# Kernel tuning notes

Measured on AMD Instinct MI355X. Metric: run time of the kernel, lower is better.

The kernel has to match this reference:

```python
import jax, jax.numpy as jnp
import numpy as np
import math

EMB_DIM = 1024
N_HEADS = 16
HEAD_DIM = EMB_DIM // N_HEADS
B, T = 4, 2048


def bitlinear(x, w):
    # BitNet b1.58 absmean ternary quantization. NOTE: the source never
    # rescales the ternary weights by `scale`, so forward uses raw {-1,0,1}.
    scale = jnp.maximum(jnp.mean(jnp.abs(w)), 1e-8)
    w_ternary = jnp.clip(jnp.round(w / scale), -1.0, 1.0)
    w_q = w + jax.lax.stop_gradient(w_ternary - w)  # STE
    return x @ w_q.T


def setup_inputs() -> dict:
    key = jax.random.key(0)
    k1, k2, k3 = jax.random.split(key, 3)
    x = jax.random.normal(k1, (B, T, EMB_DIM), dtype=jnp.float32)
    w_qkv = jax.random.normal(k2, (3 * EMB_DIM, EMB_DIM), dtype=jnp.float32) * 0.02
    w_out = jax.random.normal(k3, (EMB_DIM, EMB_DIM), dtype=jnp.float32) * 0.02
    return {"x": x, "w_qkv": w_qkv, "w_out": w_out}


def reference(x, w_qkv, w_out):
    Bc, Tc, C = x.shape
    qkv = bitlinear(x, w_qkv)  # [B, T, 3C]
    q, k, v = jnp.split(qkv, 3, axis=2)

    def split_heads(t):  # [B, T, C] -> [B, H, T, D]
        return t.reshape(Bc, Tc, N_HEADS, HEAD_DIM).transpose(0, 2, 1, 3)

    q, k, v = split_heads(q), split_heads(k), split_heads(v)
    scale = math.sqrt(HEAD_DIM)
    scores = jnp.einsum("bhqd,bhkd->bhqk", q, k) / scale  # [B, H, T, T]
    causal = jnp.triu(jnp.ones((Tc, Tc), dtype=bool), k=1)
    scores = jnp.where(causal, -jnp.inf, scores)
    attn = jax.nn.softmax(scores, axis=-1)
    out = jnp.einsum("bhqk,bhkd->bhqd", attn, v)  # [B, H, T, D]
    out = out.transpose(0, 2, 1, 3).reshape(Bc, Tc, C)
    return bitlinear(out, w_out)
```

## Files before the change

kernel.cpp:

```cpp
#include <hip/hip_runtime.h>
#include <hip/hip_bf16.h>

#define EMB   1024
#define NHEAD 16
#define HDIM  64
#define BSZ   4
#define SEQ   2048
#define MROWS (BSZ*SEQ)
#define NQKV  (3*EMB)

typedef __bf16 bf16;
typedef __bf16 bf16v4 __attribute__((ext_vector_type(4)));
typedef __bf16 bf16v8 __attribute__((ext_vector_type(8)));
typedef float  f32v4  __attribute__((ext_vector_type(4)));
typedef float  f32v16 __attribute__((ext_vector_type(16)));
typedef int    i32v4  __attribute__((ext_vector_type(4)));
typedef int    i32v16 __attribute__((ext_vector_type(16)));
typedef char   c8v4   __attribute__((ext_vector_type(4)));

#define MFMA16(a,b,c)   __builtin_amdgcn_mfma_f32_16x16x32_bf16((a),(b),(c),0,0,0)
#define MFMA32B(a,b,c)  __builtin_amdgcn_mfma_f32_32x32x16_bf16((a),(b),(c),0,0,0)
#define MFMAI8_32(a,b,c) __builtin_amdgcn_mfma_i32_32x32x32_i8((a),(b),(c),0,0,0)

__device__ __forceinline__ void gload_lds16(const void* g, void* l) {
  __builtin_amdgcn_global_load_lds((const __attribute__((address_space(1))) void*)g,
                                   (__attribute__((address_space(3))) void*)l,
                                   16, 0, 0);
}

#define DPP_FMAX(x, ctrl) do {                                                     \
    int _t = __builtin_amdgcn_update_dpp(0, __float_as_int(x), (ctrl), 0xf, 0xf, true); \
    (x) = fmaxf((x), __int_as_float(_t)); } while (0)


__global__ void abs_sum_kernel(const float4* __restrict__ w, int n4, float* out) {
  float s = 0.f;
  for (int i = blockIdx.x * blockDim.x + threadIdx.x; i < n4; i += gridDim.x * blockDim.x) {
    float4 v = w[i];
    s += fabsf(v.x) + fabsf(v.y) + fabsf(v.z) + fabsf(v.w);
  }
  #pragma unroll
  for (int off = 32; off; off >>= 1) s += __shfl_down(s, off, 64);
  __shared__ float red[4];
  int lane = threadIdx.x & 63, wid = threadIdx.x >> 6;
  if (lane == 0) red[wid] = s;
  __syncthreads();
  if (threadIdx.x == 0) atomicAdd(out, red[0] + red[1] + red[2] + red[3]);
}

__global__ void ternarize_both_kernel(const float4* __restrict__ wqkv,
                                      const float4* __restrict__ wout,
                                      const float* __restrict__ sums,
                                      c8v4* __restrict__ out8,
                                      bf16v4* __restrict__ outb) {
  int i = blockIdx.x * blockDim.x + threadIdx.x;
  const int N1_4 = (NQKV * EMB) / 4;
  if (i < N1_4) {
    float scale = fmaxf(sums[0] / (float)(NQKV * EMB), 1e-8f);
    float4 v = wqkv[i];
    c8v4 o;
    o[0] = (char)(int)fmaxf(-1.f, fminf(1.f, rintf(v.x / scale)));
    o[1] = (char)(int)fmaxf(-1.f, fminf(1.f, rintf(v.y / scale)));
    o[2] = (char)(int)fmaxf(-1.f, fminf(1.f, rintf(v.z / scale)));
    o[3] = (char)(int)fmaxf(-1.f, fminf(1.f, rintf(v.w / scale)));
    out8[i] = o;
  } else {
    int j = i - N1_4;
    float scale = fmaxf(sums[1] / (float)(EMB * EMB), 1e-8f);
    float4 v = wout[j];
    bf16v4 o;
    o[0] = (bf16)fmaxf(-1.f, fminf(1.f, rintf(v.x / scale)));
    o[1] = (bf16)fmaxf(-1.f, fminf(1.f, rintf(v.y / scale)));
    o[2] = (bf16)fmaxf(-1.f, fminf(1.f, rintf(v.z / scale)));
    o[3] = (bf16)fmaxf(-1.f, fminf(1.f, rintf(v.w / scale)));
    outb[j] = o;
  }
}

__global__ void quant_x_kernel(const float4* __restrict__ x, c8v4* __restrict__ p1,
                               c8v4* __restrict__ p2, int n4) {
  int i = blockIdx.x * blockDim.x + threadIdx.x;
  if (i >= n4) return;
  float4 v = x[i];
  c8v4 a, b;
  float vv[4] = {v.x, v.y, v.z, v.w};
  #pragma unroll
  for (int k = 0; k < 4; ++k) {
    float q1 = fminf(fmaxf(rintf(vv[k] * 16.f), -127.f), 127.f);
    float r = vv[k] - q1 * 0.0625f;
    float q2 = fminf(fmaxf(rintf(r * 4096.f), -127.f), 127.f);
    a[k] = (char)(int)q1;
    b[k] = (char)(int)q2;
  }
  p1[i] = a;
  p2[i] = b;
}


__launch_bounds__(256, 2)
__global__ void gemm_qkv_kernel(const char* __restrict__ xq1, const char* __restrict__ xq2,
                                const char* __restrict__ w8,
                                bf16* __restrict__ qh, bf16* __restrict__ ql,
                                bf16* __restrict__ kh, bf16* __restrict__ kl,
                                bf16* __restrict__ vt) {
  __shared__ __align__(16) char A1[3][128 * 64];
  __shared__ __align__(16) char A2[3][128 * 64];
  __shared__ __align__(16) char Bs[3][128 * 64];
  const int tid = threadIdx.x;
  const int lane = tid & 63, wid = tid >> 6;
  const int c31 = lane & 31, half = lane >> 5;
  const int m0 = blockIdx.x * 128, n0 = blockIdx.y * 128;
  const int wm = (wid >> 1) * 64, wn = (wid & 1) * 64;
  i32v16 acc1[2][2] = {};
  i32v16 acc2[2][2] = {};

  auto stage = [&](int bi, int kt) {
    #pragma unroll
    for (int r = 0; r < 2; ++r) {
      int li = r * 256 + tid;
      int row = li >> 2, cs = li & 3;
      int cg = cs ^ ((row >> 1) & 3);
      gload_lds16(xq1 + (size_t)(m0 + row) * EMB + kt * 64 + cg * 16, &A1[bi][li * 16]);
      gload_lds16(xq2 + (size_t)(m0 + row) * EMB + kt * 64 + cg * 16, &A2[bi][li * 16]);
      gload_lds16(w8  + (size_t)(n0 + row) * EMB + kt * 64 + cg * 16, &Bs[bi][li * 16]);
    }
  };

  stage(0, 0);
  for (int kt = 0; kt < EMB / 64; ++kt) {
    const int bi = kt % 3;
    if (kt + 1 < EMB / 64) {
      stage((kt + 1) % 3, kt + 1);
      asm volatile("s_waitcnt vmcnt(6)" ::: "memory");
    } else {
      asm volatile("s_waitcnt vmcnt(0)" ::: "memory");
    }
    __builtin_amdgcn_s_barrier();
    i32v4 a1[2][2], a2[2][2], bq[2][2];
    #pragma unroll
    for (int ks = 0; ks < 2; ++ks)
      #pragma unroll
      for (int tt = 0; tt < 2; ++tt) {
        int arow = wm + tt * 32 + c31;
        int aslot = (ks * 2 + half) ^ ((arow >> 1) & 3);
        a1[ks][tt] = *(const i32v4*)&A1[bi][arow * 64 + aslot * 16];
        a2[ks][tt] = *(const i32v4*)&A2[bi][arow * 64 + aslot * 16];
        int brow = wn + tt * 32 + c31;
        int bslot = (ks * 2 + half) ^ ((brow >> 1) & 3);
        bq[ks][tt] = *(const i32v4*)&Bs[bi][brow * 64 + bslot * 16];
      }
    #pragma unroll
    for (int ks = 0; ks < 2; ++ks)
      #pragma unroll
      for (int ti = 0; ti < 2; ++ti)
        #pragma unroll
        for (int tj = 0; tj < 2; ++tj) {
          acc1[ti][tj] = MFMAI8_32(a1[ks][ti], bq[ks][tj], acc1[ti][tj]);
          acc2[ti][tj] = MFMAI8_32(a2[ks][ti], bq[ks][tj], acc2[ti][tj]);
        }
  }
  const float S1 = 0.0625f, S2 = 1.f / 4096.f;
  const float QSCALE = 0.18033688011112042f;
  #pragma unroll
  for (int ti = 0; ti < 2; ++ti)
    #pragma unroll
    for (int tj = 0; tj < 2; ++tj) {
      const int n = n0 + wn + tj * 32 + c31;
      const int region = n >> 10, c1 = n & 1023, h = c1 >> 6, d = c1 & 63;
      #pragma unroll
      for (int g = 0; g < 4; ++g) {
        const int m_b = m0 + wm + ti * 32 + 8 * g + 4 * half;
        float c[4];
        #pragma unroll
        for (int rr = 0; rr < 4; ++rr)
          c[rr] = (float)acc1[ti][tj][g * 4 + rr] * S1 + (float)acc2[ti][tj][g * 4 + rr] * S2;
        if (region == 0) {
          #pragma unroll
          for (int rr = 0; rr < 4; ++rr) {
            int m = m_b + rr;
            int b = m >> 11, t = m & (SEQ - 1);
            size_t idx = (((size_t)(b * NHEAD + h) * SEQ + t) << 6) + d;
            float cs = c[rr] * QSCALE;
            bf16 hi = (bf16)cs;
            qh[idx] = hi; ql[idx] = (bf16)(cs - (float)hi);
          }
        } else if (region == 1) {
          #pragma unroll
          for (int rr = 0; rr < 4; ++rr) {
            int m = m_b + rr;
            int b = m >> 11, t = m & (SEQ - 1);
            size_t idx = (((size_t)(b * NHEAD + h) * SEQ + t) << 6) + d;
            bf16 hi = (bf16)c[rr];
            kh[idx] = hi; kl[idx] = (bf16)(c[rr] - (float)hi);
          }
        } else {
          bf16v4 pk;
          #pragma unroll
          for (int rr = 0; rr < 4; ++rr) pk[rr] = (bf16)c[rr];
          int b = m_b >> 11, t = m_b & (SEQ - 1);
          *(bf16v4*)&vt[((size_t)(b * NHEAD + h) * HDIM + d) * SEQ + t] = pk;
        }
      }
    }
}


__launch_bounds__(256, 2)
__global__ void attn_kernel(const bf16* __restrict__ qh, const bf16* __restrict__ ql,
                            const bf16* __restrict__ kh, const bf16* __restrict__ kl,
                            const bf16* __restrict__ vt, bf16* __restrict__ o) {
  __shared__ __align__(16) char smem[66560];
  bf16* Qh = (bf16*)smem;
  bf16* Ql = (bf16*)(smem + 16384);
  bf16* Pw = (bf16*)(smem + 49152);
  const int tid = threadIdx.x;
  const int lane = tid & 63, wid = tid >> 6;
  const int quad = lane >> 4, l16 = lane & 15;
  const int xs = l16 & 7;
  const int pair = blockIdx.x;
  const int bh = blockIdx.y;
  const size_t base = (size_t)bh * SEQ * HDIM;

  auto stage_kv = [&](char* dst, int k0) {
    #pragma unroll
    for (int r = 0; r < 2; ++r) {
      int li = r * 256 + tid;
      int srow = li >> 3, scg = (li & 7) ^ (srow & 7);
      gload_lds16(kh + base + (size_t)(k0 + srow) * HDIM + scg * 8, (bf16*)dst + (size_t)li * 8);
      gload_lds16(kl + base + (size_t)(k0 + srow) * HDIM + scg * 8, (bf16*)(dst + 8192) + (size_t)li * 8);
      gload_lds16(vt + base + (size_t)srow * SEQ + k0 + scg * 8,    (bf16*)(dst + 16384) + (size_t)li * 8);
    }
  };

  bf16v8 ones_f;
  {
    bf16 v1 = (l16 == 0) ? (bf16)1.0f : (bf16)0.0f;
    #pragma unroll
    for (int j = 0; j < 8; ++j) ones_f[j] = v1;
  }
  const int b = bh >> 4, h = bh & 15;

  for (int phase = 0; phase < 2; ++phase) {
    const int qt = phase ? (7 - pair) : (8 + pair);
    const int q0 = qt * 128;

    __syncthreads();
    #pragma unroll
    for (int r = 0; r < 4; ++r) {
      int li = r * 256 + tid;
      int row = li >> 3, cg = (li & 7) ^ (row & 7);
      gload_lds16(qh + base + (size_t)(q0 + row) * HDIM + cg * 8, &Qh[li * 8]);
      gload_lds16(ql + base + (size_t)(q0 + row) * HDIM + cg * 8, &Ql[li * 8]);
    }
    __syncthreads();
    bf16v8 qhf[2][2], qlf[2][2];
    #pragma unroll
    for (int sub = 0; sub < 2; ++sub)
      #pragma unroll
      for (int kk = 0; kk < 2; ++kk) {
        int off = (wid * 32 + sub * 16 + l16) * 64 + (((kk << 2) | quad) ^ xs) * 8;
        qhf[sub][kk] = *(const bf16v8*)&Qh[off];
        qlf[sub][kk] = *(const bf16v8*)&Ql[off];
      }
    __syncthreads();

    f32v4 oacc[2][4] = {};
    f32v4 lacc[2] = {};
    float mrow[2][4];
    #pragma unroll
    for (int s = 0; s < 2; ++s)
      #pragma unroll
      for (int r = 0; r < 4; ++r) mrow[s][r] = -1e30f;

    const int qw0 = q0 + wid * 32;
    const int qrow_hi = qw0 + 31;
    const int ntiles = 2 * qt + 2;

    stage_kv(smem, 0);

    for (int ktile = 0; ktile < ntiles; ++ktile) {
      char* cb = smem + (size_t)((ktile & 1) * 24576);
      char* nb = smem + (size_t)(((ktile + 1) & 1) * 24576);
      __syncthreads();
      if (ktile + 1 < ntiles) stage_kv(nb, (ktile + 1) * 64);
      const int k0 = ktile * 64;
      if (k0 > qrow_hi) continue;

      bf16* Kh_ = (bf16*)cb;
      bf16* Kl_ = (bf16*)(cb + 8192);
      bf16* Vt_ = (bf16*)(cb + 16384);

      f32v4 sacc[2][4] = {};
      __builtin_amdgcn_s_setprio(1);
      #pragma unroll
      for (int kk = 0; kk < 2; ++kk) {
        const int co = (((kk << 2) | quad) ^ xs) * 8;
        bf16v8 khf[4], klf[4];
        #pragma unroll
        for (int nt = 0; nt < 4; ++nt) {
          khf[nt] = *(const bf16v8*)&Kh_[(nt * 16 + l16) * 64 + co];
          klf[nt] = *(const bf16v8*)&Kl_[(nt * 16 + l16) * 64 + co];
        }
        #pragma unroll
        for (int sub = 0; sub < 2; ++sub)
          #pragma unroll
          for (int nt = 0; nt < 4; ++nt) {
            sacc[sub][nt] = MFMA16(qhf[sub][kk], khf[nt], sacc[sub][nt]);
            sacc[sub][nt] = MFMA16(qhf[sub][kk], klf[nt], sacc[sub][nt]);
            sacc[sub][nt] = MFMA16(qlf[sub][kk], khf[nt], sacc[sub][nt]);
          }
      }
      __builtin_amdgcn_s_setprio(0);

      #pragma unroll
      for (int sub = 0; sub < 2; ++sub) {
        if (k0 > qw0 + sub * 16 + 15) continue;
        const int qrow_base = qw0 + sub * 16 + quad * 4;
        #pragma unroll
        for (int nt = 0; nt < 4; ++nt) {
          int key = k0 + nt * 16 + l16;
          #pragma unroll
          for (int r = 0; r < 4; ++r)
            if (key > qrow_base + r) sacc[sub][nt][r] = -1e30f;
        }
        float alpha[4];
        #pragma unroll
        for (int r = 0; r < 4; ++r) {
          float mx = fmaxf(fmaxf(sacc[sub][0][r], sacc[sub][1][r]),
                           fmaxf(sacc[sub][2][r], sacc[sub][3][r]));
          DPP_FMAX(mx, 0x128);
          DPP_FMAX(mx, 0x124);
          DPP_FMAX(mx, 0x122);
          DPP_FMAX(mx, 0x121);
          float mnew = fmaxf(mrow[sub][r], mx);
          alpha[r] = __builtin_amdgcn_exp2f(mrow[sub][r] - mnew);
          mrow[sub][r] = mnew;
        }
        bf16* pwave = Pw + (wid * 2 + sub) * (16 * 68);
        #pragma unroll
        for (int nt = 0; nt < 4; ++nt)
          #pragma unroll
          for (int r = 0; r < 4; ++r)
            pwave[(quad * 4 + r) * 68 + nt * 16 + l16] =
                (bf16)__builtin_amdgcn_exp2f(sacc[sub][nt][r] - mrow[sub][r]);
        #pragma unroll
        for (int r = 0; r < 4; ++r) {
          lacc[sub][r] *= alpha[r];
          #pragma unroll
          for (int dt = 0; dt < 4; ++dt) oacc[sub][dt][r] *= alpha[r];
        }
      }

      __builtin_amdgcn_s_setprio(1);
      #pragma unroll
      for (int kk = 0; kk < 2; ++kk) {
        const int co = (((kk << 2) | quad) ^ xs) * 8;
        bf16v8 vf[4];
        #pragma unroll
        for (int dt = 0; dt < 4; ++dt)
          vf[dt] = *(const bf16v8*)&Vt_[(dt * 16 + l16) * 64 + co];
        #pragma unroll
        for (int sub = 0; sub < 2; ++sub) {
          if (k0 > qw0 + sub * 16 + 15) continue;
          bf16v8 pf = *(const bf16v8*)&Pw[(wid * 2 + sub) * (16 * 68) + l16 * 68 + kk * 32 + quad * 8];
          lacc[sub] = MFMA16(pf, ones_f, lacc[sub]);
          #pragma unroll
          for (int dt = 0; dt < 4; ++dt)
            oacc[sub][dt] = MFMA16(pf, vf[dt], oacc[sub][dt]);
        }
      }
      __builtin_amdgcn_s_setprio(0);
    }

    #pragma unroll
    for (int sub = 0; sub < 2; ++sub) {
      float lrow[4];
      #pragma unroll
      for (int r = 0; r < 4; ++r) lrow[r] = __shfl(lacc[sub][r], lane & 48, 64);
      #pragma unroll
      for (int dt = 0; dt < 4; ++dt)
        #pragma unroll
        for (int r = 0; r < 4; ++r) {
          int q = q0 + wid * 32 + sub * 16 + quad * 4 + r;
          int d = dt * 16 + l16;
          float val = oacc[sub][dt][r] / lrow[r];
          o[((size_t)(b * SEQ + q)) * EMB + h * HDIM + d] = (bf16)val;
        }
    }
  }
}


__launch_bounds__(256, 2)
__global__ void gemm_out_kernel(const bf16* __restrict__ oin, const bf16* __restrict__ wt,
                                float* __restrict__ out) {
  __shared__ __align__(16) bf16 As_[4][128 * 32];
  __shared__ __align__(16) bf16 Bs_[4][128 * 32];
  const int tid = threadIdx.x;
  const int lane = tid & 63, wid = tid >> 6;
  const int c31 = lane & 31, half = lane >> 5;
  const int m0 = blockIdx.x * 128, n0 = blockIdx.y * 128;
  const int wm = (wid >> 1) * 64, wn = (wid & 1) * 64;
  f32v16 acc[2][2] = {};
  const int NT = EMB / 32;

  auto stage = [&](int bi, int kt) {
    #pragma unroll
    for (int r = 0; r < 2; ++r) {
      int li = r * 256 + tid;
      int row = li >> 2, cs = li & 3;
      int cg = cs ^ ((row >> 1) & 3);
      gload_lds16(oin + (size_t)(m0 + row) * EMB + kt * 32 + cg * 8, &As_[bi][li * 8]);
      gload_lds16(wt  + (size_t)(n0 + row) * EMB + kt * 32 + cg * 8, &Bs_[bi][li * 8]);
    }
  };

  stage(0, 0);
  stage(1, 1);
  for (int kt = 0; kt < NT; ++kt) {
    const int bi = kt & 3;
    if (kt + 2 < NT) {
      stage((kt + 2) & 3, kt + 2);
      asm volatile("s_waitcnt vmcnt(8)" ::: "memory");
    } else if (kt + 1 < NT) {
      asm volatile("s_waitcnt vmcnt(4)" ::: "memory");
    } else {
      asm volatile("s_waitcnt vmcnt(0)" ::: "memory");
    }
    __builtin_amdgcn_s_barrier();
    bf16v8 af[2][2], bq[2][2];
    #pragma unroll
    for (int ks = 0; ks < 2; ++ks)
      #pragma unroll
      for (int tt = 0; tt < 2; ++tt) {
        int arow = wm + tt * 32 + c31;
        int aslot = (2 * ks + half) ^ ((arow >> 1) & 3);
        af[ks][tt] = *(const bf16v8*)&As_[bi][arow * 32 + aslot * 8];
        int brow = wn + tt * 32 + c31;
        int bslot = (2 * ks + half) ^ ((brow >> 1) & 3);
        bq[ks][tt] = *(const bf16v8*)&Bs_[bi][brow * 32 + bslot * 8];
      }
    #pragma unroll
    for (int ks = 0; ks < 2; ++ks)
      #pragma unroll
      for (int ti = 0; ti < 2; ++ti)
        #pragma unroll
        for (int tj = 0; tj < 2; ++tj)
          acc[ti][tj] = MFMA32B(af[ks][ti], bq[ks][tj], acc[ti][tj]);
  }
  #pragma unroll
  for (int ti = 0; ti < 2; ++ti)
    #pragma unroll
    for (int tj = 0; tj < 2; ++tj) {
      const int n = n0 + wn + tj * 32 + c31;
      #pragma unroll
      for (int g = 0; g < 4; ++g) {
        const int m_b = m0 + wm + ti * 32 + 8 * g + 4 * half;
        #pragma unroll
        for (int rr = 0; rr < 4; ++rr)
          out[(size_t)(m_b + rr) * EMB + n] = acc[ti][tj][g * 4 + rr];
      }
    }
}


extern "C" void kernel_launch(void* const* d_in, const int* in_sizes, int n_in,
                              void* d_out, int out_size, void* d_ws, size_t ws_size,
                              hipStream_t stream) {
  const float* x     = (const float*)d_in[0];
  const float* w_qkv = (const float*)d_in[1];
  const float* w_out = (const float*)d_in[2];
  float* out = (float*)d_out;
  char* ws = (char*)d_ws;

  const size_t SZ  = (size_t)MROWS * EMB * sizeof(bf16);
  const size_t SZ8 = (size_t)MROWS * EMB;
  size_t off = 0;
  float* sums = (float*)ws;            off = 256;
  char*  wq8  = (char*)(ws + off);     off += (size_t)NQKV * EMB;
  bf16*  wo_t = (bf16*)(ws + off);     off += (size_t)EMB * EMB * sizeof(bf16);
  char*  xq1  = (char*)(ws + off);     off += SZ8;
  char*  xq2  = (char*)(ws + off);     off += SZ8;
  bf16*  qh   = (bf16*)(ws + off);     off += SZ;
  bf16*  ql   = (bf16*)(ws + off);     off += SZ;
  bf16*  kh   = (bf16*)(ws + off);     off += SZ;
  bf16*  kl   = (bf16*)(ws + off);     off += SZ;
  bf16*  vt   = (bf16*)(ws + off);     off += SZ;
  bf16*  ob   = (bf16*)xq1;
  (void)in_sizes; (void)n_in; (void)out_size; (void)ws_size;

  hipMemsetAsync(sums, 0, 2 * sizeof(float), stream);
  abs_sum_kernel<<<256, 256, 0, stream>>>((const float4*)w_qkv, (NQKV * EMB) / 4, &sums[0]);
  abs_sum_kernel<<<256, 256, 0, stream>>>((const float4*)w_out, (EMB * EMB) / 4, &sums[1]);
  ternarize_both_kernel<<<(NQKV * EMB + EMB * EMB) / 1024, 256, 0, stream>>>(
      (const float4*)w_qkv, (const float4*)w_out, sums, (c8v4*)wq8, (bf16v4*)wo_t);
  quant_x_kernel<<<(MROWS * EMB) / 1024, 256, 0, stream>>>(
      (const float4*)x, (c8v4*)xq1, (c8v4*)xq2, (MROWS * EMB) / 4);
  gemm_qkv_kernel<<<dim3(MROWS / 128, NQKV / 128), 256, 0, stream>>>(xq1, xq2, wq8, qh, ql, kh, kl, vt);
  attn_kernel<<<dim3(8, BSZ * NHEAD), 256, 0, stream>>>(qh, ql, kh, kl, vt, ob);
  gemm_out_kernel<<<dim3(MROWS / 128, EMB / 128), 256, 0, stream>>>(ob, wo_t, out);
}
```

Before: 315.5 us.

## Deepen GEMM prefetch distance and merge weight/activation prep kernels

Both GEMM kernels now prefetch one stage further ahead. QKV goes to distance 2 over its 3 LDS buffers, and the output projection goes to distance 3 over its 4 buffers. The next-stage load is issued after the barrier, so the buffer being overwritten is known to have been fully read. Separately, the two abs-sum launches are merged into one grid, and the x quantization and weight ternarization are merged into one prep kernel, cutting kernel launches. Keeping more loads in flight should hide more global-memory latency, at the cost of more outstanding memory traffic per block.

```diff
diff --git a/kernel.cpp b/kernel.cpp
--- a/kernel.cpp
+++ b/kernel.cpp
@@ -33,9 +33,16 @@
     (x) = fmaxf((x), __int_as_float(_t)); } while (0)
 
 
-__global__ void abs_sum_kernel(const float4* __restrict__ w, int n4, float* out) {
+__global__ void abs_sum2_kernel(const float4* __restrict__ wq, int nq4,
+                                const float4* __restrict__ wo, int no4,
+                                float* __restrict__ sums) {
+  const bool second = blockIdx.x >= 256;
+  const float4* w = second ? wo : wq;
+  const int n4 = second ? no4 : nq4;
+  float* out = second ? &sums[1] : &sums[0];
+  const int bid = second ? blockIdx.x - 256 : blockIdx.x;
   float s = 0.f;
-  for (int i = blockIdx.x * blockDim.x + threadIdx.x; i < n4; i += gridDim.x * blockDim.x) {
+  for (int i = bid * blockDim.x + threadIdx.x; i < n4; i += 256 * blockDim.x) {
     float4 v = w[i];
     s += fabsf(v.x) + fabsf(v.y) + fabsf(v.z) + fabsf(v.w);
   }
@@ -48,52 +55,51 @@
   if (threadIdx.x == 0) atomicAdd(out, red[0] + red[1] + red[2] + red[3]);
 }
 
-__global__ void ternarize_both_kernel(const float4* __restrict__ wqkv,
-                                      const float4* __restrict__ wout,
-                                      const float* __restrict__ sums,
-                                      c8v4* __restrict__ out8,
-                                      bf16v4* __restrict__ outb) {
-  int i = blockIdx.x * blockDim.x + threadIdx.x;
-  const int N1_4 = (NQKV * EMB) / 4;
-  if (i < N1_4) {
-    float scale = fmaxf(sums[0] / (float)(NQKV * EMB), 1e-8f);
-    float4 v = wqkv[i];
-    c8v4 o;
-    o[0] = (char)(int)fmaxf(-1.f, fminf(1.f, rintf(v.x / scale)));
-    o[1] = (char)(int)fmaxf(-1.f, fminf(1.f, rintf(v.y / scale)));
-    o[2] = (char)(int)fmaxf(-1.f, fminf(1.f, rintf(v.z / scale)));
-    o[3] = (char)(int)fmaxf(-1.f, fminf(1.f, rintf(v.w / scale)));
-    out8[i] = o;
+__global__ void prep_kernel(const float4* __restrict__ x, c8v4* __restrict__ p1,
+                            c8v4* __restrict__ p2,
+                            const float4* __restrict__ wqkv, const float4* __restrict__ wout,
+                            const float* __restrict__ sums,
+                            c8v4* __restrict__ out8, bf16v4* __restrict__ outb) {
+  const int QB = (MROWS * EMB) / 1024;
+  if (blockIdx.x < QB) {
+    int i = blockIdx.x * blockDim.x + threadIdx.x;
+    float4 v = x[i];
+    c8v4 a, b;
+    float vv[4] = {v.x, v.y, v.z, v.w};
+    #pragma unroll
+    for (int k = 0; k < 4; ++k) {
+      float q1 = fminf(fmaxf(rintf(vv[k] * 16.f), -127.f), 127.f);
+      float r = vv[k] - q1 * 0.0625f;
+      float q2 = fminf(fmaxf(rintf(r * 4096.f), -127.f), 127.f);
+      a[k] = (char)(int)q1;
+      b[k] = (char)(int)q2;
+    }
+    p1[i] = a;
+    p2[i] = b;
   } else {
-    int j = i - N1_4;
-    float scale = fmaxf(sums[1] / (float)(EMB * EMB), 1e-8f);
-    float4 v = wout[j];
-    bf16v4 o;
-    o[0] = (bf16)fmaxf(-1.f, fminf(1.f, rintf(v.x / scale)));
-    o[1] = (bf16)fmaxf(-1.f, fminf(1.f, rintf(v.y / scale)));
-    o[2] = (bf16)fmaxf(-1.f, fminf(1.f, rintf(v.z / scale)));
-    o[3] = (bf16)fmaxf(-1.f, fminf(1.f, rintf(v.w / scale)));
-    outb[j] = o;
+    int i = (blockIdx.x - QB) * blockDim.x + threadIdx.x;
+    const int N1_4 = (NQKV * EMB) / 4;
+    if (i < N1_4) {
+      float scale = fmaxf(sums[0] / (float)(NQKV * EMB), 1e-8f);
+      float4 v = wqkv[i];
+      c8v4 o;
+      o[0] = (char)(int)fmaxf(-1.f, fminf(1.f, rintf(v.x / scale)));
+      o[1] = (char)(int)fmaxf(-1.f, fminf(1.f, rintf(v.y / scale)));
+      o[2] = (char)(int)fmaxf(-1.f, fminf(1.f, rintf(v.z / scale)));
+      o[3] = (char)(int)fmaxf(-1.f, fminf(1.f, rintf(v.w / scale)));
+      out8[i] = o;
+    } else {
+      int j = i - N1_4;
+      float scale = fmaxf(sums[1] / (float)(EMB * EMB), 1e-8f);
+      float4 v = wout[j];
+      bf16v4 o;
+      o[0] = (bf16)fmaxf(-1.f, fminf(1.f, rintf(v.x / scale)));
+      o[1] = (bf16)fmaxf(-1.f, fminf(1.f, rintf(v.y / scale)));
+      o[2] = (bf16)fmaxf(-1.f, fminf(1.f, rintf(v.z / scale)));
+      o[3] = (bf16)fmaxf(-1.f, fminf(1.f, rintf(v.w / scale)));
+      outb[j] = o;
+    }
   }
-}
-
-__global__ void quant_x_kernel(const float4* __restrict__ x, c8v4* __restrict__ p1,
-                               c8v4* __restrict__ p2, int n4) {
-  int i = blockIdx.x * blockDim.x + threadIdx.x;
-  if (i >= n4) return;
-  float4 v = x[i];
-  c8v4 a, b;
-  float vv[4] = {v.x, v.y, v.z, v.w};
-  #pragma unroll
-  for (int k = 0; k < 4; ++k) {
-    float q1 = fminf(fmaxf(rintf(vv[k] * 16.f), -127.f), 127.f);
-    float r = vv[k] - q1 * 0.0625f;
-    float q2 = fminf(fmaxf(rintf(r * 4096.f), -127.f), 127.f);
-    a[k] = (char)(int)q1;
-    b[k] = (char)(int)q2;
-  }
-  p1[i] = a;
-  p2[i] = b;
 }
 
 
@@ -127,15 +133,16 @@
   };
 
   stage(0, 0);
+  stage(1, 1);
   for (int kt = 0; kt < EMB / 64; ++kt) {
     const int bi = kt % 3;
     if (kt + 1 < EMB / 64) {
-      stage((kt + 1) % 3, kt + 1);
       asm volatile("s_waitcnt vmcnt(6)" ::: "memory");
     } else {
       asm volatile("s_waitcnt vmcnt(0)" ::: "memory");
     }
     __builtin_amdgcn_s_barrier();
+    if (kt + 2 < EMB / 64) stage((kt + 2) % 3, kt + 2);
     i32v4 a1[2][2], a2[2][2], bq[2][2];
     #pragma unroll
     for (int ks = 0; ks < 2; ++ks)
@@ -417,10 +424,10 @@
 
   stage(0, 0);
   stage(1, 1);
+  stage(2, 2);
   for (int kt = 0; kt < NT; ++kt) {
     const int bi = kt & 3;
     if (kt + 2 < NT) {
-      stage((kt + 2) & 3, kt + 2);
       asm volatile("s_waitcnt vmcnt(8)" ::: "memory");
     } else if (kt + 1 < NT) {
       asm volatile("s_waitcnt vmcnt(4)" ::: "memory");
@@ -428,6 +435,7 @@
       asm volatile("s_waitcnt vmcnt(0)" ::: "memory");
     }
     __builtin_amdgcn_s_barrier();
+    if (kt + 3 < NT) stage((kt + 3) & 3, kt + 3);
     bf16v8 af[2][2], bq[2][2];
     #pragma unroll
     for (int ks = 0; ks < 2; ++ks)
@@ -490,12 +498,11 @@
   (void)in_sizes; (void)n_in; (void)out_size; (void)ws_size;
 
   hipMemsetAsync(sums, 0, 2 * sizeof(float), stream);
-  abs_sum_kernel<<<256, 256, 0, stream>>>((const float4*)w_qkv, (NQKV * EMB) / 4, &sums[0]);
-  abs_sum_kernel<<<256, 256, 0, stream>>>((const float4*)w_out, (EMB * EMB) / 4, &sums[1]);
-  ternarize_both_kernel<<<(NQKV * EMB + EMB * EMB) / 1024, 256, 0, stream>>>(
+  abs_sum2_kernel<<<512, 256, 0, stream>>>((const float4*)w_qkv, (NQKV * EMB) / 4,
+                                           (const float4*)w_out, (EMB * EMB) / 4, sums);
+  prep_kernel<<<(MROWS * EMB) / 1024 + (NQKV * EMB + EMB * EMB) / 1024, 256, 0, stream>>>(
+      (const float4*)x, (c8v4*)xq1, (c8v4*)xq2,
       (const float4*)w_qkv, (const float4*)w_out, sums, (c8v4*)wq8, (bf16v4*)wo_t);
-  quant_x_kernel<<<(MROWS * EMB) / 1024, 256, 0, stream>>>(
-      (const float4*)x, (c8v4*)xq1, (c8v4*)xq2, (MROWS * EMB) / 4);
   gemm_qkv_kernel<<<dim3(MROWS / 128, NQKV / 128), 256, 0, stream>>>(xq1, xq2, wq8, qh, ql, kh, kl, vt);
   attn_kernel<<<dim3(8, BSZ * NHEAD), 256, 0, stream>>>(qh, ql, kh, kl, vt, ob);
   gemm_out_kernel<<<dim3(MROWS / 128, EMB / 128), 256, 0, stream>>>(ob, wo_t, out);
```

Result: no change. 311.2 us (-1.4%).
